# Optimization experiments

Hardware: AMD Instinct MI355X
Metric: run time of the kernel (lower is better)

## Reference

```python
import jax, jax.numpy as jnp
import numpy as np

LN_EPS = 1e-5

def _prelu(x, a):
    return jnp.where(x > 0, x, a * x)

def setup_inputs() -> dict:
    key = jax.random.key(0)
    ks = jax.random.split(key, 16)
    C, NH, HD = 256, 8, 32
    s = lambda k, shape, scale: jax.random.normal(k, shape, jnp.float32) * scale
    return {
        "x":   s(ks[0], (1, C, 48, 48), 1.0),
        "Wq":  s(ks[1], (NH, HD, C), 1.0 / np.sqrt(C)),
        "bq":  s(ks[2], (NH, HD), 0.02),
        "Wk":  s(ks[3], (NH, HD, C), 1.0 / np.sqrt(C)),
        "bk":  s(ks[4], (NH, HD), 0.02),
        "Wv":  s(ks[5], (NH, HD, C), 1.0 / np.sqrt(C)),
        "bv":  s(ks[6], (NH, HD), 0.02),
        "Wfc": s(ks[7], (C, C), 1.0 / np.sqrt(C)),
        "bfc": s(ks[8], (C,), 0.02),
        "w1":  s(ks[9], (C // 16, C), 1.0 / np.sqrt(C)),
        "b1":  s(ks[10], (C // 16,), 0.02),
        "a1":  jnp.full((1,), 0.25, jnp.float32),
        "w2":  s(ks[11], (C, C // 16), 1.0 / np.sqrt(C // 16)),
        "b2":  s(ks[12], (C,), 0.02),
        "a2":  jnp.full((1,), 0.25, jnp.float32),
    }

def _mha(xs, Wq, bq, Wk, bk, Wv, bv, Wfc, bfc):
    # xs: [B, C, Hs, Ws]; all heads batched into one einsum per projection
    B, C, Hs, Ws = xs.shape
    N = Hs * Ws
    xf = xs.reshape(B, C, N)
    q = jnp.einsum('bcn,hdc->bhnd', xf, Wq) + bq[None, :, None, :]
    k = jnp.einsum('bcn,hdc->bhnd', xf, Wk) + bk[None, :, None, :]
    v = jnp.einsum('bcn,hdc->bhnd', xf, Wv) + bv[None, :, None, :]
    # unscaled scores, softmax over keys (matches torch.bmm(q,k) + softmax dim=-1)
    attn = jax.nn.softmax(jnp.einsum('bhnd,bhmd->bhnm', q, k), axis=-1)
    o = jnp.einsum('bhnm,bhmd->bhnd', attn, v)          # [B, H, N, D]
    o = o.transpose(0, 1, 3, 2).reshape(B, C, Hs, Ws)   # concat heads along C
    return jnp.einsum('bchw,oc->bohw', o, Wfc) + bfc[None, :, None, None]

def reference(x, Wq, bq, Wk, bk, Wv, bv, Wfc, bfc, w1, b1, a1, w2, b2, a2):
    B, C, H, W = x.shape
    num_scales = 4
    out = jnp.zeros_like(x)
    for i in range(num_scales):
        Hs, Ws = H // (2 ** i), W // (2 ** i)
        xs = jax.image.resize(x, (B, C, Hs, Ws), 'bilinear', antialias=False)
        y = _mha(xs, Wq, bq, Wk, bk, Wv, bv, Wfc, bfc)
        out = out + jax.image.resize(y, (B, C, H, W), 'bilinear', antialias=False)
    # SE channel gating
    avg = out.mean(axis=(2, 3))                         # [B, C]
    h = _prelu(avg @ w1.T + b1, a1)
    cw = jax.nn.sigmoid(h @ w2.T + b2)                  # [B, C]
    out = out * cw[:, :, None, None] + x
    # layer_norm over (C, H, W), no affine
    mu = out.mean(axis=(1, 2, 3), keepdims=True)
    var = out.var(axis=(1, 2, 3), keepdims=True)
    out = (out - mu) * jax.lax.rsqrt(var + LN_EPS)
    out = _prelu(out, a2)
    # dropout is identity in eval mode
    return out
```

## Files before the change

kernel.cpp:

```cpp
#include <hip/hip_runtime.h>
#include <hip/hip_bf16.h>

#define NTOT 3060
#define NPIX 2304
#define CH   256
#define NLN  589824
#define VSTR 3072

#define P0_OFF   0
#define P1_OFF   2359296
#define PM0_OFF  2654208
#define PL0_OFF  2727936
#define PM1_OFF  2801664
#define PL1_OFF  2810880

typedef __attribute__((ext_vector_type(8))) short bf16x8;
typedef __attribute__((ext_vector_type(16))) float f32x16;

__device__ __forceinline__ bf16x8 ldfrag(const unsigned short* p) {
  int4 v = *reinterpret_cast<const int4*>(p);
  return __builtin_bit_cast(bf16x8, v);
}
__device__ __forceinline__ unsigned f2bf(float f) {
  unsigned u = __builtin_bit_cast(unsigned, f);
  return (u + 0x7FFFu + ((u >> 16) & 1u)) >> 16;
}
__device__ __forceinline__ unsigned pk2(float a, float b) {
  return f2bf(a) | (f2bf(b) << 16);
}
#define MFMA32(a, b, c) __builtin_amdgcn_mfma_f32_32x32x16_bf16((a), (b), (c), 0, 0, 0)

__global__ __launch_bounds__(256) void k_castW(const float* __restrict__ Wq,
                                               const float* __restrict__ Wk,
                                               const float* __restrict__ Wv,
                                               const float* __restrict__ Wfc,
                                               unsigned* __restrict__ Wb) {
  int i = blockIdx.x * 256 + threadIdx.x;
  int m = i >> 15;
  int r = i & 32767;
  const float* src = (m == 0) ? Wq : (m == 1) ? Wk : (m == 2) ? Wv : Wfc;
  float2 v = *(const float2*)&src[(size_t)r * 2];
  Wb[i] = pk2(v.x, v.y);
}

__global__ __launch_bounds__(256) void k_downsample(const float* __restrict__ x,
                                                    unsigned short* __restrict__ xsT) {
  int t = threadIdx.x;
  int n = blockIdx.x * 64 + (t & 63);
  int cb = blockIdx.y * 64 + (t >> 6) * 16;
  if (n >= NTOT) return;
  int p, Ws, s;
  if (n < 2304)      { s = 0; p = n;        Ws = 48; }
  else if (n < 2880) { s = 1; p = n - 2304; Ws = 24; }
  else if (n < 3024) { s = 2; p = n - 2880; Ws = 12; }
  else               { s = 3; p = n - 3024; Ws = 6;  }
  int oy = p / Ws, ox = p - oy * Ws;
  int b0; bool avg = (s != 0);
  if (s == 0) b0 = p;
  else {
    int r, cc;
    if (s == 1)      { r = 2 * oy;     cc = 2 * ox;     }
    else if (s == 2) { r = 4 * oy + 1; cc = 4 * ox + 1; }
    else             { r = 8 * oy + 3; cc = 8 * ox + 3; }
    b0 = r * 48 + cc;
  }
#pragma unroll
  for (int i0 = 0; i0 < 16; i0 += 8) {
    unsigned u[4];
#pragma unroll
    for (int jj = 0; jj < 4; jj++) {
      float v[2];
#pragma unroll
      for (int e = 0; e < 2; e++) {
        int c = cb + i0 + jj * 2 + e;
        const float* xc = x + (size_t)c * NPIX;
        v[e] = avg ? 0.25f * (xc[b0] + xc[b0 + 1] + xc[b0 + 48] + xc[b0 + 49])
                   : xc[b0];
      }
      u[jj] = pk2(v[0], v[1]);
    }
    *(int4*)&xsT[(size_t)n * 256 + cb + i0] = make_int4((int)u[0], (int)u[1],
                                                        (int)u[2], (int)u[3]);
  }
}

__global__ __launch_bounds__(256) void k_qkv_mfma(const unsigned short* __restrict__ Wb,
                                                  const float* __restrict__ bq,
                                                  const float* __restrict__ bk,
                                                  const float* __restrict__ bv,
                                                  const unsigned short* __restrict__ xsT,
                                                  unsigned short* __restrict__ Qbf,
                                                  unsigned short* __restrict__ Kbf,
                                                  unsigned short* __restrict__ Vt) {
  int z = blockIdx.z, h = blockIdx.y;
  int j0 = h * 32;
  const unsigned short* W = Wb + (size_t)z * 65536;
  const float* bias = (z == 0) ? bq : (z == 1) ? bk : bv;
  int t = threadIdx.x, w = t >> 6, l = t & 63, lq = l & 31, h2 = l >> 5;
  int n = blockIdx.x * 128 + w * 32 + lq;
  int nc = min(n, NTOT - 1);

  bf16x8 bfr[16];
#pragma unroll
  for (int kk = 0; kk < 16; kk++)
    bfr[kk] = ldfrag(&xsT[(size_t)nc * 256 + kk * 16 + h2 * 8]);

  f32x16 acc = {0,0,0,0,0,0,0,0,0,0,0,0,0,0,0,0};
#pragma unroll
  for (int kk = 0; kk < 16; kk++) {
    bf16x8 af = ldfrag(&W[(size_t)(j0 + lq) * 256 + kk * 16 + h2 * 8]);
    acc = MFMA32(af, bfr[kk], acc);
  }

  float4 bi[4];
#pragma unroll
  for (int g = 0; g < 4; g++) bi[g] = *(const float4*)&bias[j0 + 4 * h2 + 8 * g];

  if (n < NTOT) {
    if (z < 2) {
      unsigned short* dst = ((z == 0) ? Qbf : Kbf) + ((size_t)h * NTOT + n) * 32;
#pragma unroll
      for (int g = 0; g < 4; g++) {
        unsigned p0 = pk2(acc[4 * g + 0] + bi[g].x, acc[4 * g + 1] + bi[g].y);
        unsigned p1 = pk2(acc[4 * g + 2] + bi[g].z, acc[4 * g + 3] + bi[g].w);
        *(int2*)&dst[4 * h2 + 8 * g] = make_int2((int)p0, (int)p1);
      }
    } else {
#pragma unroll
      for (int g = 0; g < 4; g++) {
        float bb[4] = {bi[g].x, bi[g].y, bi[g].z, bi[g].w};
#pragma unroll
        for (int q = 0; q < 4; q++) {
          int d = 4 * h2 + 8 * g + q;
          Vt[(size_t)(j0 + d) * VSTR + n] = (unsigned short)f2bf(acc[4 * g + q] + bb[q]);
        }
      }
    }
  }
}

__global__ __launch_bounds__(256) void k_attn_mfma(const unsigned short* __restrict__ Qbf,
                                                   const unsigned short* __restrict__ Kbf,
                                                   const unsigned short* __restrict__ Vt,
                                                   unsigned short* __restrict__ Obf,
                                                   float* __restrict__ Pb) {
  const int Ns_tab[4]  = {2304, 576, 144, 36};
  const int off_tab[4] = {0, 2304, 2880, 3024};

  int bid = blockIdx.x;
  int sc, head, qt, sp, nsp;
  if (bid < 576)      { int qtb = bid >> 2; sp = bid & 3;  nsp = 4; sc = 0; head = qtb / 18; qt = qtb - head * 18; }
  else if (bid < 656) { int b = bid - 576; int qtb = b >> 1; sp = b & 1; nsp = 2; sc = 1; head = qtb / 5; qt = qtb - head * 5; }
  else if (bid < 672) { int b = bid - 656; sc = 2; head = b >> 1; qt = b & 1; sp = 0; nsp = 1; }
  else                { sc = 3; head = bid - 672; qt = 0; sp = 0; nsp = 1; }

  int Ns = Ns_tab[sc], off = off_tab[sc];
  int t = threadIdx.x;
  int w = t >> 6, l = t & 63;
  int lq = l & 31, h2 = l >> 5;
  int qbase = qt * 128 + w * 32;
  if (qbase >= Ns) return;

  int chunk = Ns / nsp;
  int kbeg = sp * chunk, kend = kbeg + chunk;

  const unsigned short* Qh = Qbf + ((size_t)head * NTOT + off) * 32;
  const unsigned short* Kh = Kbf + ((size_t)head * NTOT + off) * 32;
  const unsigned short* Vh = Vt + (size_t)(head * 32) * VSTR + off;

  int qc = qbase + lq; if (qc >= Ns) qc = Ns - 1;
  const unsigned short* Qp = Qh + (size_t)qc * 32 + h2 * 8;
  bf16x8 qf0 = ldfrag(Qp);
  bf16x8 qf1 = ldfrag(Qp + 16);

  float m = -3.0e38f, L = 0.f;
  f32x16 oacc = {0,0,0,0,0,0,0,0,0,0,0,0,0,0,0,0};

  int mt0 = kbeg + lq; if (mt0 >= Ns) mt0 = Ns - 1;
  const unsigned short* Kp0 = Kh + (size_t)mt0 * 32 + h2 * 8;
  bf16x8 kf0n = ldfrag(Kp0);
  bf16x8 kf1n = ldfrag(Kp0 + 16);

  for (int kb = kbeg; kb < kend; kb += 32) {
    bf16x8 kf0 = kf0n, kf1 = kf1n;
    const unsigned short* Vp = Vh + (size_t)lq * VSTR + kb + h2 * 8;
    bf16x8 vf0 = ldfrag(Vp);
    bf16x8 vf1 = ldfrag(Vp + 16);
    int kb2 = kb + 32;
    if (kb2 < kend) {
      int mt = kb2 + lq; if (mt >= Ns) mt = Ns - 1;
      const unsigned short* Kp = Kh + (size_t)mt * 32 + h2 * 8;
      kf0n = ldfrag(Kp);
      kf1n = ldfrag(Kp + 16);
    }

    f32x16 sa = {0,0,0,0,0,0,0,0,0,0,0,0,0,0,0,0};
    sa = MFMA32(kf0, qf0, sa);
    sa = MFMA32(kf1, qf1, sa);

    float s[16];
#pragma unroll
    for (int r = 0; r < 16; r++) s[r] = sa[r];
    int rem = kend - kb;
    if (rem < 32) {
#pragma unroll
      for (int r = 0; r < 16; r++) {
        int ko = (r & 3) + 8 * (r >> 2) + 4 * h2;
        if (ko >= rem) s[r] = -3.0e38f;
      }
    }
    float cm = s[0];
#pragma unroll
    for (int r = 1; r < 16; r++) cm = fmaxf(cm, s[r]);
    cm = fmaxf(cm, __shfl_xor(cm, 32));
    float mn = fmaxf(m, cm);
    float scl = __expf(m - mn);
    m = mn;
    L *= scl;
#pragma unroll
    for (int r = 0; r < 16; r++) oacc[r] *= scl;

    float p[16], ls = 0.f;
#pragma unroll
    for (int r = 0; r < 16; r++) { p[r] = __expf(s[r] - m); ls += p[r]; }
    ls += __shfl_xor(ls, 32);
    L += ls;

    unsigned u[8], su[8];
#pragma unroll
    for (int g = 0; g < 8; g++) u[g] = pk2(p[2 * g], p[2 * g + 1]);
#pragma unroll
    for (int g = 0; g < 8; g++) su[g] = __shfl_xor(u[g], 32);

    int4 w0, w1;
    if (h2 == 0) {
      w0 = make_int4((int)u[0], (int)u[1], (int)su[0], (int)su[1]);
      w1 = make_int4((int)u[4], (int)u[5], (int)su[4], (int)su[5]);
    } else {
      w0 = make_int4((int)su[2], (int)su[3], (int)u[2], (int)u[3]);
      w1 = make_int4((int)su[6], (int)su[7], (int)u[6], (int)u[7]);
    }
    bf16x8 pf0 = __builtin_bit_cast(bf16x8, w0);
    bf16x8 pf1 = __builtin_bit_cast(bf16x8, w1);

    oacc = MFMA32(vf0, pf0, oacc);
    oacc = MFMA32(vf1, pf1, oacc);
  }

  int q = qbase + lq;
  if (q < Ns) {
    if (nsp == 1) {
      float rl = 1.f / L;
      unsigned short* dst = Obf + (size_t)(off + q) * 256 + head * 32;
#pragma unroll
      for (int g = 0; g < 4; g++) {
        unsigned p0 = pk2(oacc[4 * g + 0] * rl, oacc[4 * g + 1] * rl);
        unsigned p1 = pk2(oacc[4 * g + 2] * rl, oacc[4 * g + 3] * rl);
        *(int2*)&dst[4 * h2 + 8 * g] = make_int2((int)p0, (int)p1);
      }
    } else {
      int qs = (sc == 0) ? 2304 : 576;
      float* P  = (sc == 0) ? Pb + P0_OFF  : Pb + P1_OFF;
      float* Pm = (sc == 0) ? Pb + PM0_OFF : Pb + PM1_OFF;
      float* PL = (sc == 0) ? Pb + PL0_OFF : Pb + PL1_OFF;
      size_t row = (size_t)(sp * 8 + head) * qs + q;
      float* Prow = P + row * 32;
#pragma unroll
      for (int g = 0; g < 4; g++) {
        float4 v = make_float4(oacc[4 * g + 0], oacc[4 * g + 1],
                               oacc[4 * g + 2], oacc[4 * g + 3]);
        *(float4*)&Prow[g * 8 + 4 * h2] = v;
      }
      if (h2 == 0) { Pm[row] = m; PL[row] = L; }
    }
  }
}

__global__ __launch_bounds__(256) void k_combine(const float* __restrict__ Pb,
                                                 unsigned short* __restrict__ Obf) {
  int tid = blockIdx.x * 256 + threadIdx.x;
  int h, q, off, nsp, qs;
  const float* P; const float* Pm; const float* PL;
  if (tid < 18432) {
    h = tid / 2304; q = tid - h * 2304; off = 0; nsp = 4; qs = 2304;
    P = Pb + P0_OFF; Pm = Pb + PM0_OFF; PL = Pb + PL0_OFF;
  } else if (tid < 23040) {
    int b = tid - 18432;
    h = b / 576; q = b - h * 576; off = 2304; nsp = 2; qs = 576;
    P = Pb + P1_OFF; Pm = Pb + PM1_OFF; PL = Pb + PL1_OFF;
  } else return;

  float mv[4], lv[4];
  float M = -3.0e38f;
  for (int s = 0; s < nsp; s++) {
    size_t row = (size_t)(s * 8 + h) * qs + q;
    mv[s] = Pm[row]; lv[s] = PL[row];
    M = fmaxf(M, mv[s]);
  }
  float e[4], denom = 0.f;
  for (int s = 0; s < nsp; s++) { e[s] = __expf(mv[s] - M); denom += e[s] * lv[s]; }
  float rden = 1.f / denom;

  unsigned short* dst = Obf + (size_t)(off + q) * 256 + h * 32;
#pragma unroll
  for (int d4 = 0; d4 < 8; d4++) {
    float4 acc = make_float4(0.f, 0.f, 0.f, 0.f);
    for (int s = 0; s < nsp; s++) {
      size_t row = (size_t)(s * 8 + h) * qs + q;
      float4 v = *(const float4*)&P[row * 32 + d4 * 4];
      acc.x += e[s] * v.x; acc.y += e[s] * v.y;
      acc.z += e[s] * v.z; acc.w += e[s] * v.w;
    }
    unsigned p0 = pk2(acc.x * rden, acc.y * rden);
    unsigned p1 = pk2(acc.z * rden, acc.w * rden);
    *(int2*)&dst[d4 * 4] = make_int2((int)p0, (int)p1);
  }
}

__global__ __launch_bounds__(256) void k_fc_mfma(const unsigned short* __restrict__ Wfcb,
                                                 const float* __restrict__ bfc,
                                                 const unsigned short* __restrict__ Obf,
                                                 float* __restrict__ Yb) {
  int j0 = blockIdx.y * 32;
  int t = threadIdx.x, w = t >> 6, l = t & 63, lq = l & 31, h2 = l >> 5;
  int n = blockIdx.x * 128 + w * 32 + lq;
  int nc = min(n, NTOT - 1);

  bf16x8 bfr[16];
#pragma unroll
  for (int kk = 0; kk < 16; kk++)
    bfr[kk] = ldfrag(&Obf[(size_t)nc * 256 + kk * 16 + h2 * 8]);

  f32x16 acc = {0,0,0,0,0,0,0,0,0,0,0,0,0,0,0,0};
#pragma unroll
  for (int kk = 0; kk < 16; kk++) {
    bf16x8 af = ldfrag(&Wfcb[(size_t)(j0 + lq) * 256 + kk * 16 + h2 * 8]);
    acc = MFMA32(af, bfr[kk], acc);
  }

  float4 bi[4];
#pragma unroll
  for (int g = 0; g < 4; g++) bi[g] = *(const float4*)&bfc[j0 + 4 * h2 + 8 * g];

  if (n < NTOT) {
#pragma unroll
    for (int g = 0; g < 4; g++) {
      float bb[4] = {bi[g].x, bi[g].y, bi[g].z, bi[g].w};
#pragma unroll
      for (int q = 0; q < 4; q++) {
        int d = 4 * h2 + 8 * g + q;
        Yb[(size_t)(j0 + d) * NTOT + n] = acc[4 * g + q] + bb[q];
      }
    }
  }
}

__device__ __forceinline__ float bil4(const float* __restrict__ a, int S,
                                      int y, int x, float scale, float tr) {
  float fy = fmaf((float)y, scale, tr);
  float fx = fmaf((float)x, scale, tr);
  int iy = (int)floorf(fy); float wy = fy - (float)iy;
  int ix = (int)floorf(fx); float wx = fx - (float)ix;
  int y0 = min(max(iy, 0), S - 1);
  int y1 = min(max(iy + 1, 0), S - 1);
  int x0 = min(max(ix, 0), S - 1);
  int x1 = min(max(ix + 1, 0), S - 1);
  float v00 = a[y0 * S + x0], v01 = a[y0 * S + x1];
  float v10 = a[y1 * S + x0], v11 = a[y1 * S + x1];
  float top = v00 + wx * (v01 - v00);
  float bot = v10 + wx * (v11 - v10);
  return top + wy * (bot - top);
}

__global__ __launch_bounds__(256) void k_upacc(const float* __restrict__ Y,
                                               float* __restrict__ outa) {
  int idx = blockIdx.x * 256 + threadIdx.x;
  if (idx >= NLN) return;
  int c = idx / NPIX;
  int p = idx - c * NPIX;
  int y = p / 48, x = p - y * 48;
  const float* Yc = Y + c * NTOT;
  float v = Yc[p];
  v += bil4(Yc + 2304, 24, y, x, 0.5f,   -0.25f);
  v += bil4(Yc + 2880, 12, y, x, 0.25f,  -0.375f);
  v += bil4(Yc + 3024, 6,  y, x, 0.125f, -0.4375f);
  outa[idx] = v;
}

__global__ __launch_bounds__(256) void k_chanstats(const float* __restrict__ outa,
                                                   const float* __restrict__ x,
                                                   float* __restrict__ st) {
  int c = blockIdx.x, t = threadIdx.x;
  float so = 0.f, soo = 0.f, sox = 0.f, sx = 0.f, sxx = 0.f;
  for (int p = t; p < NPIX; p += 256) {
    float o  = outa[c * NPIX + p];
    float xv = x[c * NPIX + p];
    so += o; soo += o * o; sox += o * xv; sx += xv; sxx += xv * xv;
  }
#pragma unroll
  for (int off = 32; off > 0; off >>= 1) {
    so  += __shfl_down(so, off, 64);
    soo += __shfl_down(soo, off, 64);
    sox += __shfl_down(sox, off, 64);
    sx  += __shfl_down(sx, off, 64);
    sxx += __shfl_down(sxx, off, 64);
  }
  __shared__ float part[4][5];
  int wv = t >> 6;
  if ((t & 63) == 0) {
    part[wv][0] = so; part[wv][1] = soo; part[wv][2] = sox;
    part[wv][3] = sx; part[wv][4] = sxx;
  }
  __syncthreads();
  if (t == 0) {
    float a0 = 0.f, a1 = 0.f, a2 = 0.f, a3 = 0.f, a4 = 0.f;
#pragma unroll
    for (int wi = 0; wi < 4; wi++) {
      a0 += part[wi][0]; a1 += part[wi][1]; a2 += part[wi][2];
      a3 += part[wi][3]; a4 += part[wi][4];
    }
    st[c] = a0; st[256 + c] = a1; st[512 + c] = a2; st[768 + c] = a3; st[1024 + c] = a4;
  }
}

__global__ __launch_bounds__(256) void k_se(const float* __restrict__ st,
                                            const float* __restrict__ w1,
                                            const float* __restrict__ b1,
                                            const float* __restrict__ a1,
                                            const float* __restrict__ w2,
                                            const float* __restrict__ b2,
                                            float* __restrict__ cw,
                                            float* __restrict__ scal) {
  __shared__ float avg_s[256];
  __shared__ float h_s[16];
  __shared__ float rS[4], rSS[4];
  int t = threadIdx.x;
  float avg = st[t] * (1.f / (float)NPIX);
  avg_s[t] = avg;
  __syncthreads();
  int i = t >> 4, pp = t & 15;
  float partial = 0.f;
  for (int c = pp; c < 256; c += 16) partial += avg_s[c] * w1[i * 256 + c];
#pragma unroll
  for (int off = 8; off > 0; off >>= 1) partial += __shfl_down(partial, off, 16);
  if (pp == 0) {
    float hv = partial + b1[i];
    float al = a1[0];
    h_s[i] = hv > 0.f ? hv : al * hv;
  }
  __syncthreads();
  float s2 = b2[t];
#pragma unroll
  for (int k = 0; k < 16; k++) s2 += h_s[k] * w2[t * 16 + k];
  float cwv = 1.f / (1.f + expf(-s2));
  cw[t] = cwv;

  float S_part  = cwv * st[t] + st[768 + t];
  float SS_part = cwv * cwv * st[256 + t] + 2.f * cwv * st[512 + t] + st[1024 + t];
#pragma unroll
  for (int off = 32; off > 0; off >>= 1) {
    S_part  += __shfl_down(S_part, off, 64);
    SS_part += __shfl_down(SS_part, off, 64);
  }
  if ((t & 63) == 0) { rS[t >> 6] = S_part; rSS[t >> 6] = SS_part; }
  __syncthreads();
  if (t == 0) {
    float S = rS[0] + rS[1] + rS[2] + rS[3];
    float SS = rSS[0] + rSS[1] + rSS[2] + rSS[3];
    float mu = S / (float)NLN;
    float var = SS / (float)NLN - mu * mu;
    scal[0] = mu;
    scal[1] = rsqrtf(var + 1e-5f);
  }
}

__global__ __launch_bounds__(256) void k_final(const float* __restrict__ outa,
                                               const float* __restrict__ x,
                                               const float* __restrict__ cw,
                                               const float* __restrict__ scal,
                                               const float* __restrict__ a2,
                                               float* __restrict__ out) {
  int idx = blockIdx.x * 256 + threadIdx.x;
  if (idx >= NLN) return;
  int c = idx / NPIX;
  float g = outa[idx] * cw[c] + x[idx];
  float v = (g - scal[0]) * scal[1];
  float al = a2[0];
  out[idx] = v > 0.f ? v : al * v;
}

extern "C" void kernel_launch(void* const* d_in, const int* in_sizes, int n_in,
                              void* d_out, int out_size, void* d_ws, size_t ws_size,
                              hipStream_t stream) {
  const float* x   = (const float*)d_in[0];
  const float* Wq  = (const float*)d_in[1];
  const float* bq  = (const float*)d_in[2];
  const float* Wk  = (const float*)d_in[3];
  const float* bk  = (const float*)d_in[4];
  const float* Wv  = (const float*)d_in[5];
  const float* bv  = (const float*)d_in[6];
  const float* Wfc = (const float*)d_in[7];
  const float* bfc = (const float*)d_in[8];
  const float* w1  = (const float*)d_in[9];
  const float* b1  = (const float*)d_in[10];
  const float* a1  = (const float*)d_in[11];
  const float* w2  = (const float*)d_in[12];
  const float* b2  = (const float*)d_in[13];
  const float* a2  = (const float*)d_in[14];

  float* ws = (float*)d_ws;
  unsigned short* xsT = (unsigned short*)ws;
  float* Pb = ws;
  unsigned short* Obf = (unsigned short*)(ws + 3133440);
  unsigned short* Wb  = (unsigned short*)(ws + 3525120);
  unsigned short* Qbf = (unsigned short*)(ws + 3916800);
  unsigned short* Kbf = Qbf + 783360;
  float* Yb = ws + 3916800;
  unsigned short* Vt = (unsigned short*)(ws + 4700160);
  float* outa = ws + 4700160;
  float* st   = ws + 5289984;
  float* cwv  = ws + 5291264;
  float* scal = ws + 5291520;

  k_castW<<<dim3(512), 256, 0, stream>>>(Wq, Wk, Wv, Wfc, (unsigned*)Wb);
  k_downsample<<<dim3(48, 4), 256, 0, stream>>>(x, xsT);
  k_qkv_mfma<<<dim3(24, 8, 3), 256, 0, stream>>>(Wb, bq, bk, bv, xsT, Qbf, Kbf, Vt);
  k_attn_mfma<<<dim3(680), 256, 0, stream>>>(Qbf, Kbf, Vt, Obf, Pb);
  k_combine<<<dim3(90), 256, 0, stream>>>(Pb, Obf);
  k_fc_mfma<<<dim3(24, 8), 256, 0, stream>>>(Wb + 196608, bfc, Obf, Yb);
  k_upacc<<<dim3(NLN / 256), 256, 0, stream>>>(Yb, outa);
  k_chanstats<<<dim3(256), 256, 0, stream>>>(outa, x, st);
  k_se<<<dim3(1), 256, 0, stream>>>(st, w1, b1, a1, w2, b2, cwv, scal);
  k_final<<<dim3(NLN / 256), 256, 0, stream>>>(outa, x, cwv, scal, a2, (float*)d_out);
}
```

Before: 173.5 us.

## Double attention key splits, fuse pre-kernels, and fuse upsample with channel stats

```diff
diff --git a/kernel.cpp b/kernel.cpp
--- a/kernel.cpp
+++ b/kernel.cpp
@@ -7,12 +7,23 @@
 #define NLN  589824
 #define VSTR 3072
 
-#define P0_OFF   0
-#define P1_OFF   2359296
-#define PM0_OFF  2654208
-#define PL0_OFF  2727936
-#define PM1_OFF  2801664
-#define PL1_OFF  2810880
+#define XST_OFF   0
+#define WB_OFF    400000
+#define QBF_OFF   600000
+#define KBF_OFF   1000000
+#define VT_OFF    1400000
+#define OBF_OFF   1800000
+#define YB_OFF    2200000
+#define OUTA_OFF  3000000
+#define ST_OFF    3600000
+#define CW_OFF    3601280
+#define SCAL_OFF  3601536
+#define P0_OFF    4000000
+#define PM0_OFF   8718592
+#define PL0_OFF   8866048
+#define P1_OFF    9100000
+#define PM1_OFF   9700000
+#define PL1_OFF   9718432
 
 typedef __attribute__((ext_vector_type(8))) short bf16x8;
 typedef __attribute__((ext_vector_type(16))) float f32x16;
@@ -30,24 +41,26 @@
 }
 #define MFMA32(a, b, c) __builtin_amdgcn_mfma_f32_32x32x16_bf16((a), (b), (c), 0, 0, 0)
 
-__global__ __launch_bounds__(256) void k_castW(const float* __restrict__ Wq,
-                                               const float* __restrict__ Wk,
-                                               const float* __restrict__ Wv,
-                                               const float* __restrict__ Wfc,
-                                               unsigned* __restrict__ Wb) {
-  int i = blockIdx.x * 256 + threadIdx.x;
-  int m = i >> 15;
-  int r = i & 32767;
-  const float* src = (m == 0) ? Wq : (m == 1) ? Wk : (m == 2) ? Wv : Wfc;
-  float2 v = *(const float2*)&src[(size_t)r * 2];
-  Wb[i] = pk2(v.x, v.y);
-}
-
-__global__ __launch_bounds__(256) void k_downsample(const float* __restrict__ x,
-                                                    unsigned short* __restrict__ xsT) {
-  int t = threadIdx.x;
-  int n = blockIdx.x * 64 + (t & 63);
-  int cb = blockIdx.y * 64 + (t >> 6) * 16;
+__global__ __launch_bounds__(256) void k_pre(const float* __restrict__ Wq,
+                                             const float* __restrict__ Wk,
+                                             const float* __restrict__ Wv,
+                                             const float* __restrict__ Wfc,
+                                             const float* __restrict__ x,
+                                             unsigned* __restrict__ Wb,
+                                             unsigned short* __restrict__ xsT) {
+  int b = blockIdx.x, t = threadIdx.x;
+  if (b < 512) {
+    int i = b * 256 + t;
+    int m = i >> 15;
+    int r = i & 32767;
+    const float* src = (m == 0) ? Wq : (m == 1) ? Wk : (m == 2) ? Wv : Wfc;
+    float2 v = *(const float2*)&src[(size_t)r * 2];
+    Wb[i] = pk2(v.x, v.y);
+    return;
+  }
+  int bx = b - 512;
+  int n = (bx % 48) * 64 + (t & 63);
+  int cb = (bx / 48) * 64 + (t >> 6) * 16;
   if (n >= NTOT) return;
   int p, Ws, s;
   if (n < 2304)      { s = 0; p = n;        Ws = 48; }
@@ -143,16 +156,16 @@
                                                    const unsigned short* __restrict__ Kbf,
                                                    const unsigned short* __restrict__ Vt,
                                                    unsigned short* __restrict__ Obf,
-                                                   float* __restrict__ Pb) {
+                                                   float* __restrict__ wsf) {
   const int Ns_tab[4]  = {2304, 576, 144, 36};
   const int off_tab[4] = {0, 2304, 2880, 3024};
 
   int bid = blockIdx.x;
   int sc, head, qt, sp, nsp;
-  if (bid < 576)      { int qtb = bid >> 2; sp = bid & 3;  nsp = 4; sc = 0; head = qtb / 18; qt = qtb - head * 18; }
-  else if (bid < 656) { int b = bid - 576; int qtb = b >> 1; sp = b & 1; nsp = 2; sc = 1; head = qtb / 5; qt = qtb - head * 5; }
-  else if (bid < 672) { int b = bid - 656; sc = 2; head = b >> 1; qt = b & 1; sp = 0; nsp = 1; }
-  else                { sc = 3; head = bid - 672; qt = 0; sp = 0; nsp = 1; }
+  if (bid < 1152)      { int qtb = bid >> 3; sp = bid & 7; nsp = 8; sc = 0; head = qtb / 18; qt = qtb - head * 18; }
+  else if (bid < 1312) { int b = bid - 1152; int qtb = b >> 2; sp = b & 3; nsp = 4; sc = 1; head = qtb / 5; qt = qtb - head * 5; }
+  else if (bid < 1328) { int b = bid - 1312; sc = 2; head = b >> 1; qt = b & 1; sp = 0; nsp = 1; }
+  else                 { sc = 3; head = bid - 1328; qt = 0; sp = 0; nsp = 1; }
 
   int Ns = Ns_tab[sc], off = off_tab[sc];
   int t = threadIdx.x;
@@ -260,9 +273,9 @@
       }
     } else {
       int qs = (sc == 0) ? 2304 : 576;
-      float* P  = (sc == 0) ? Pb + P0_OFF  : Pb + P1_OFF;
-      float* Pm = (sc == 0) ? Pb + PM0_OFF : Pb + PM1_OFF;
-      float* PL = (sc == 0) ? Pb + PL0_OFF : Pb + PL1_OFF;
+      float* P  = (sc == 0) ? wsf + P0_OFF  : wsf + P1_OFF;
+      float* Pm = (sc == 0) ? wsf + PM0_OFF : wsf + PM1_OFF;
+      float* PL = (sc == 0) ? wsf + PL0_OFF : wsf + PL1_OFF;
       size_t row = (size_t)(sp * 8 + head) * qs + q;
       float* Prow = P + row * 32;
 #pragma unroll
@@ -276,28 +289,28 @@
   }
 }
 
-__global__ __launch_bounds__(256) void k_combine(const float* __restrict__ Pb,
+__global__ __launch_bounds__(256) void k_combine(const float* __restrict__ wsf,
                                                  unsigned short* __restrict__ Obf) {
   int tid = blockIdx.x * 256 + threadIdx.x;
   int h, q, off, nsp, qs;
   const float* P; const float* Pm; const float* PL;
   if (tid < 18432) {
-    h = tid / 2304; q = tid - h * 2304; off = 0; nsp = 4; qs = 2304;
-    P = Pb + P0_OFF; Pm = Pb + PM0_OFF; PL = Pb + PL0_OFF;
+    h = tid / 2304; q = tid - h * 2304; off = 0; nsp = 8; qs = 2304;
+    P = wsf + P0_OFF; Pm = wsf + PM0_OFF; PL = wsf + PL0_OFF;
   } else if (tid < 23040) {
     int b = tid - 18432;
-    h = b / 576; q = b - h * 576; off = 2304; nsp = 2; qs = 576;
-    P = Pb + P1_OFF; Pm = Pb + PM1_OFF; PL = Pb + PL1_OFF;
+    h = b / 576; q = b - h * 576; off = 2304; nsp = 4; qs = 576;
+    P = wsf + P1_OFF; Pm = wsf + PM1_OFF; PL = wsf + PL1_OFF;
   } else return;
 
-  float mv[4], lv[4];
+  float mv[8], lv[8];
   float M = -3.0e38f;
   for (int s = 0; s < nsp; s++) {
     size_t row = (size_t)(s * 8 + h) * qs + q;
     mv[s] = Pm[row]; lv[s] = PL[row];
     M = fmaxf(M, mv[s]);
   }
-  float e[4], denom = 0.f;
+  float e[8], denom = 0.f;
   for (int s = 0; s < nsp; s++) { e[s] = __expf(mv[s] - M); denom += e[s] * lv[s]; }
   float rden = 1.f / denom;
 
@@ -372,30 +385,25 @@
   return top + wy * (bot - top);
 }
 
-__global__ __launch_bounds__(256) void k_upacc(const float* __restrict__ Y,
-                                               float* __restrict__ outa) {
-  int idx = blockIdx.x * 256 + threadIdx.x;
-  if (idx >= NLN) return;
-  int c = idx / NPIX;
-  int p = idx - c * NPIX;
-  int y = p / 48, x = p - y * 48;
-  const float* Yc = Y + c * NTOT;
-  float v = Yc[p];
-  v += bil4(Yc + 2304, 24, y, x, 0.5f,   -0.25f);
-  v += bil4(Yc + 2880, 12, y, x, 0.25f,  -0.375f);
-  v += bil4(Yc + 3024, 6,  y, x, 0.125f, -0.4375f);
-  outa[idx] = v;
-}
-
-__global__ __launch_bounds__(256) void k_chanstats(const float* __restrict__ outa,
-                                                   const float* __restrict__ x,
-                                                   float* __restrict__ st) {
+__global__ __launch_bounds__(256) void k_upstats(const float* __restrict__ Yb,
+                                                 const float* __restrict__ x,
+                                                 float* __restrict__ outa,
+                                                 float* __restrict__ st) {
   int c = blockIdx.x, t = threadIdx.x;
+  const float* Yc = Yb + (size_t)c * NTOT;
+  const float* xc = x + (size_t)c * NPIX;
   float so = 0.f, soo = 0.f, sox = 0.f, sx = 0.f, sxx = 0.f;
-  for (int p = t; p < NPIX; p += 256) {
-    float o  = outa[c * NPIX + p];
-    float xv = x[c * NPIX + p];
-    so += o; soo += o * o; sox += o * xv; sx += xv; sxx += xv * xv;
+#pragma unroll
+  for (int i = 0; i < 9; i++) {
+    int p = t + i * 256;
+    int y = p / 48, xx = p - y * 48;
+    float v = Yc[p];
+    v += bil4(Yc + 2304, 24, y, xx, 0.5f,   -0.25f);
+    v += bil4(Yc + 2880, 12, y, xx, 0.25f,  -0.375f);
+    v += bil4(Yc + 3024, 6,  y, xx, 0.125f, -0.4375f);
+    outa[(size_t)c * NPIX + p] = v;
+    float xv = xc[p];
+    so += v; soo += v * v; sox += v * xv; sx += xv; sxx += xv * xv;
   }
 #pragma unroll
   for (int off = 32; off > 0; off >>= 1) {
@@ -508,28 +516,25 @@
   const float* b2  = (const float*)d_in[13];
   const float* a2  = (const float*)d_in[14];
 
-  float* ws = (float*)d_ws;
-  unsigned short* xsT = (unsigned short*)ws;
-  float* Pb = ws;
-  unsigned short* Obf = (unsigned short*)(ws + 3133440);
-  unsigned short* Wb  = (unsigned short*)(ws + 3525120);
-  unsigned short* Qbf = (unsigned short*)(ws + 3916800);
-  unsigned short* Kbf = Qbf + 783360;
-  float* Yb = ws + 3916800;
-  unsigned short* Vt = (unsigned short*)(ws + 4700160);
-  float* outa = ws + 4700160;
-  float* st   = ws + 5289984;
-  float* cwv  = ws + 5291264;
-  float* scal = ws + 5291520;
-
-  k_castW<<<dim3(512), 256, 0, stream>>>(Wq, Wk, Wv, Wfc, (unsigned*)Wb);
-  k_downsample<<<dim3(48, 4), 256, 0, stream>>>(x, xsT);
+  float* wsf = (float*)d_ws;
+  unsigned short* xsT = (unsigned short*)(wsf + XST_OFF);
+  unsigned short* Wb  = (unsigned short*)(wsf + WB_OFF);
+  unsigned short* Qbf = (unsigned short*)(wsf + QBF_OFF);
+  unsigned short* Kbf = (unsigned short*)(wsf + KBF_OFF);
+  unsigned short* Vt  = (unsigned short*)(wsf + VT_OFF);
+  unsigned short* Obf = (unsigned short*)(wsf + OBF_OFF);
+  float* Yb   = wsf + YB_OFF;
+  float* outa = wsf + OUTA_OFF;
+  float* st   = wsf + ST_OFF;
+  float* cwv  = wsf + CW_OFF;
+  float* scal = wsf + SCAL_OFF;
+
+  k_pre<<<dim3(704), 256, 0, stream>>>(Wq, Wk, Wv, Wfc, x, (unsigned*)Wb, xsT);
   k_qkv_mfma<<<dim3(24, 8, 3), 256, 0, stream>>>(Wb, bq, bk, bv, xsT, Qbf, Kbf, Vt);
-  k_attn_mfma<<<dim3(680), 256, 0, stream>>>(Qbf, Kbf, Vt, Obf, Pb);
-  k_combine<<<dim3(90), 256, 0, stream>>>(Pb, Obf);
+  k_attn_mfma<<<dim3(1336), 256, 0, stream>>>(Qbf, Kbf, Vt, Obf, wsf);
+  k_combine<<<dim3(90), 256, 0, stream>>>(wsf, Obf);
   k_fc_mfma<<<dim3(24, 8), 256, 0, stream>>>(Wb + 196608, bfc, Obf, Yb);
-  k_upacc<<<dim3(NLN / 256), 256, 0, stream>>>(Yb, outa);
-  k_chanstats<<<dim3(256), 256, 0, stream>>>(outa, x, st);
+  k_upstats<<<dim3(256), 256, 0, stream>>>(Yb, x, outa, st);
   k_se<<<dim3(1), 256, 0, stream>>>(st, w1, b1, a1, w2, b2, cwv, scal);
   k_final<<<dim3(NLN / 256), 256, 0, stream>>>(outa, x, cwv, scal, a2, (float*)d_out);
 }
```

Measured after the change: 174.0 us. Within noise of the previous version (+0.3%).
